# Performance work log

Measured on AMD Instinct MI355X. Metric: run time of the kernel, lower is better.

## Reference

```python
import jax, jax.numpy as jnp
import numpy as np

MLOG32 = float(np.log(32.0))


def _maxpool(x, k):
    # F.max_pool2d(stride=1, padding=k//2) pads with -inf, matching init value
    pad = k // 2
    return jax.lax.reduce_window(x, -jnp.inf, jax.lax.max, (1, 1, k, k), (1, 1, 1, 1),
                                 ((0, 0), (0, 0), (pad, pad), (pad, pad)))


def _minpool(x, k):
    return -_maxpool(-x, k)


def _local_sum(x, k):
    # conv2d with all-ones kxk kernel, zero padding, same spatial size
    pad = k // 2
    return jax.lax.reduce_window(x, 0.0, jax.lax.add, (1, 1, k, k), (1, 1, 1, 1),
                                 ((0, 0), (0, 0), (pad, pad), (pad, pad)))


def _conv3(x, kern):
    # torch conv2d == cross-correlation == lax conv (no kernel flip)
    return jax.lax.conv_general_dilated(x, kern, (1, 1), ((1, 1), (1, 1)),
                                        dimension_numbers=('NCHW', 'OIHW', 'NCHW'))


def _otsu(gray, bins=32):
    # vectorized per-batch Otsu threshold; gray in [0,1]
    B, _, H, W = gray.shape
    v = gray.reshape(B, -1)
    idx = jnp.clip((v * bins).astype(jnp.int32), 0, bins - 1)  # histc semantics, v==1 -> last bin
    hist = jax.vmap(lambda i: jnp.bincount(i, length=bins))(idx).astype(gray.dtype)
    p = hist / (H * W + 1e-6)
    xs = jnp.linspace(0.0, 1.0, bins, dtype=gray.dtype)
    omega = jnp.cumsum(p, axis=1)
    mu = jnp.cumsum(p * xs[None, :], axis=1)
    mu_t = mu[:, -1:]
    sigma_b2 = (mu_t * omega - mu) ** 2 / (omega * (1.0 - omega) + 1e-8)
    kbest = jnp.argmax(sigma_b2, axis=1)
    edges = jnp.linspace(0.0, 1.0, bins + 1, dtype=gray.dtype)
    return edges[kbest].reshape(B, 1, 1, 1)


def _concept_maps(image_rgb, cell_dilate=10, k_local=9):
    r, g, b = image_rgb[:, 0:1], image_rgb[:, 1:2], image_rgb[:, 2:3]
    gray = jnp.clip(0.5 * (0.299 * r + 0.587 * g + 0.114 * b + 1.0), 0.0, 1.0)
    thr = _otsu(gray)
    nuc = (gray <= thr).astype(gray.dtype)
    # morphological open+close, k=3
    e = _minpool(nuc, 3)
    d = _maxpool(e, 3)
    d = _maxpool(d, 3)
    e2 = _minpool(d, 3)
    nuc = (e2 > 0.5).astype(gray.dtype)
    er = _minpool(nuc, 3)
    boundary = jnp.maximum(nuc - er, 0.0)
    lap_k = jnp.array([[0, 1, 0], [1, -4, 1], [0, 1, 0]], dtype=gray.dtype).reshape(1, 1, 3, 3)
    lap = jnp.abs(_conv3(nuc, lap_k))
    den = _local_sum(boundary, 5) + 1e-6
    roughness = lap * boundary / den
    kx = jnp.array([[1, 0, -1], [2, 0, -2], [1, 0, -1]], dtype=gray.dtype).reshape(1, 1, 3, 3)
    ky = jnp.array([[1, 2, 1], [0, 0, 0], [-1, -2, -1]], dtype=gray.dtype).reshape(1, 1, 3, 3)
    gx = _conv3(gray, kx)
    gy = _conv3(gray, ky)
    ang = jnp.arctan2(gy, gx)
    den_orient = _local_sum(jnp.ones_like(gray), k_local) + 1e-6
    ms = _local_sum(jnp.sin(ang), k_local) / den_orient
    mc = _local_sum(jnp.cos(ang), k_local) / den_orient
    circ_var = 1.0 - jnp.sqrt(ms ** 2 + mc ** 2 + 1e-6)
    kd = cell_dilate if cell_dilate % 2 == 1 else cell_dilate + 1  # force odd
    cell = jnp.minimum(_maxpool(nuc, kd), 1.0)
    A_n = _local_sum(nuc, k_local)
    A_c = jnp.maximum(_local_sum(cell, k_local) - A_n, 1.0)
    nc = A_n / A_c
    g2 = _local_sum(gray * gray, k_local) / den_orient
    g1 = _local_sum(gray, k_local) / den_orient
    ent_like = jnp.log1p(jnp.maximum(g2 - g1 * g1, 0.0))
    z_maps = jnp.concatenate([roughness, circ_var, nc, ent_like], axis=1)
    return z_maps, nuc


def _energy_forward(image_rgb, cal_a, cal_b, alpha_logits, tau_p, Ht, Wt):
    z_maps, nuc = _concept_maps(image_rgb)
    z0 = jnp.log1p(jnp.maximum(z_maps[:, 0:1], 0.0))
    z1 = jnp.clip(z_maps[:, 1:2], 0.0, 1.0)
    z2 = jnp.log1p(jnp.maximum(z_maps[:, 2:3], 0.0))
    z3 = jnp.clip(z_maps[:, 3:4], 0.0, MLOG32)
    z_stable = jnp.concatenate([z0, z1, z2, z3], axis=1)
    z_cal = jax.nn.softplus(cal_a)[None, :, None, None] * z_stable + cal_b[None, :, None, None]
    alpha = jax.nn.softmax(alpha_logits)[None, :, None, None]
    E = jnp.sum(alpha * z_cal, axis=1, keepdims=True)
    B = E.shape[0]
    if (E.shape[2], E.shape[3]) != (Ht, Wt):
        E_t = jax.image.resize(E, (B, 1, Ht, Wt), method='linear')
    else:
        E_t = E
    tau = 0.2 + jax.nn.softplus(tau_p)
    A = jax.nn.softmax((-E_t / tau).reshape(B, 1, Ht * Wt), axis=-1).reshape(B, 1, Ht, Wt)
    return A, z_maps, nuc, E_t


def setup_inputs() -> dict:
    key = jax.random.key(0)
    k1, k2, k3, k4 = jax.random.split(key, 4)
    B, H, W = 16, 512, 512
    image_rgb = 2.0 * jax.random.uniform(k1, (B, 3, H, W), dtype=jnp.float32) - 1.0
    cal_a = 1.0 + 0.1 * jax.random.normal(k2, (4,), jnp.float32)
    cal_b = 0.1 * jax.random.normal(k3, (4,), jnp.float32)
    alpha_logits = 0.1 * jax.random.normal(k4, (4,), jnp.float32)
    tau_p = jnp.float32(0.5)
    return {"image_rgb": image_rgb, "cal_a": cal_a, "cal_b": cal_b,
            "alpha_logits": alpha_logits, "tau_p": tau_p, "target_h": 512, "target_w": 512}


def reference(image_rgb, cal_a, cal_b, alpha_logits, tau_p, target_h, target_w):
    return _energy_forward(image_rgb, cal_a, cal_b, alpha_logits, tau_p, int(target_h), int(target_w))
```

## Files before the change

kernel.cpp:

```cpp
#include <hip/hip_runtime.h>
#include <math.h>
#include <stdint.h>

#define HW 512
#define IMG (HW*HW)
#define MLOG32f 3.4657359027997265f

__device__ __forceinline__ float grayf(float r, float g, float b) {
    float t = __fadd_rn(__fadd_rn(__fmul_rn(0.299f, r), __fmul_rn(0.587f, g)), __fmul_rn(0.114f, b));
    float s = __fmul_rn(0.5f, __fadd_rn(t, 1.0f));
    return fminf(fmaxf(s, 0.0f), 1.0f);
}

__device__ __forceinline__ float softplusf(float x) {
    return fmaxf(x, 0.0f) + log1pf(expf(-fabsf(x)));
}

__device__ __forceinline__ float frcp(float x)  { return __builtin_amdgcn_rcpf(x); }
__device__ __forceinline__ float frsq(float x)  { return __builtin_amdgcn_rsqf(x); }
__device__ __forceinline__ float flog1p(float x){ return __logf(1.0f + x); }

__device__ __forceinline__ uint64_t kmask(int lo, int hi) {
    return (1ull << hi) - (1ull << lo);
}

__global__ __launch_bounds__(256) void k_gray_hist(const float* __restrict__ img,
                                                   float* __restrict__ gray,
                                                   int* __restrict__ hist) {
    __shared__ int lh[32];
    int tid = threadIdx.x;
    int b = blockIdx.y;
    if (tid < 32) lh[tid] = 0;
    __syncthreads();
    const float4* rp = (const float4*)(img + (size_t)b * 3 * IMG);
    const float4* gp = (const float4*)(img + (size_t)b * 3 * IMG + IMG);
    const float4* bp = (const float4*)(img + (size_t)b * 3 * IMG + 2 * IMG);
    float4* op = (float4*)(gray + (size_t)b * IMG);
    int i = blockIdx.x * 256 + tid;
    float4 r = rp[i], g = gp[i], bb = bp[i];
    float4 o;
    o.x = grayf(r.x, g.x, bb.x);
    o.y = grayf(r.y, g.y, bb.y);
    o.z = grayf(r.z, g.z, bb.z);
    o.w = grayf(r.w, g.w, bb.w);
    op[i] = o;
    int idx[4];
    idx[0] = min(max((int)(o.x * 32.0f), 0), 31);
    idx[1] = min(max((int)(o.y * 32.0f), 0), 31);
    idx[2] = min(max((int)(o.z * 32.0f), 0), 31);
    idx[3] = min(max((int)(o.w * 32.0f), 0), 31);
    int lane = tid & 63;
    int bin = lane & 31;
    int cnt = 0;
    #pragma unroll
    for (int e = 0; e < 4; e++) {
        int v = idx[e];
        unsigned long long m0 = __ballot((v & 1)  != 0);
        unsigned long long m1 = __ballot((v & 2)  != 0);
        unsigned long long m2 = __ballot((v & 4)  != 0);
        unsigned long long m3 = __ballot((v & 8)  != 0);
        unsigned long long m4 = __ballot((v & 16) != 0);
        unsigned long long mm = (bin & 1)  ? m0 : ~m0;
        mm &= (bin & 2)  ? m1 : ~m1;
        mm &= (bin & 4)  ? m2 : ~m2;
        mm &= (bin & 8)  ? m3 : ~m3;
        mm &= (bin & 16) ? m4 : ~m4;
        cnt += __popcll(mm);
    }
    if (lane < 32) atomicAdd(&lh[bin], cnt);
    __syncthreads();
    if (tid < 32) atomicAdd(&hist[b * 32 + tid], lh[tid]);
}

__global__ void k_otsu_sc(const int* __restrict__ hist,
                          const float* __restrict__ cal_a, const float* __restrict__ cal_b,
                          const float* __restrict__ alpha_logits, const float* __restrict__ tau_p,
                          float* __restrict__ thr, float* __restrict__ sc, int B) {
    int tid = threadIdx.x;
    if (tid < B) {
        const int* h = hist + tid * 32;
        float omega[32], mu[32];
        float co = 0.0f, cm = 0.0f;
        for (int k = 0; k < 32; k++) {
            float pk = (float)h[k] * (1.0f / 262144.0f);
            float xs = (float)((double)k / 31.0);
            co += pk;
            cm += pk * xs;
            omega[k] = co; mu[k] = cm;
        }
        float mu_t = mu[31];
        float best = -1e30f; int kb = 0;
        for (int k = 0; k < 32; k++) {
            float t = mu_t * omega[k] - mu[k];
            float sb = (t * t) / (omega[k] * (1.0f - omega[k]) + 1e-8f);
            if (sb > best) { best = sb; kb = k; }
        }
        thr[tid] = (float)kb * 0.03125f;
    }
    if (tid == 63) {
        float al[4];
        float m = -1e30f;
        for (int c = 0; c < 4; c++) { al[c] = alpha_logits[c]; m = fmaxf(m, al[c]); }
        float e[4]; float s = 0.0f;
        for (int c = 0; c < 4; c++) { e[c] = expf(al[c] - m); s += e[c]; }
        float bias = 0.0f;
        for (int c = 0; c < 4; c++) {
            float alpha = e[c] / s;
            sc[c] = alpha * softplusf(cal_a[c]);
            bias += alpha * cal_b[c];
        }
        sc[4] = bias;
        float tau = 0.2f + softplusf(tau_p[0]);
        sc[5] = tau;
        sc[6] = -1.0f / tau;
    }
}

__global__ __launch_bounds__(256) void k_thresh(const float* __restrict__ gray,
                                                const float* __restrict__ thr,
                                                uint32_t* __restrict__ packed) {
    int b = blockIdx.y;
    int i = blockIdx.x * 256 + threadIdx.x;
    float t = thr[b];
    float v = gray[(size_t)b * IMG + i];
    unsigned long long m = __ballot(v <= t);
    if ((threadIdx.x & 63) == 0)
        *(uint64_t*)&packed[(size_t)b * 8192 + (i >> 5)] = m;
}

__global__ __launch_bounds__(256) void k_morph(const uint32_t* __restrict__ p0,
                                               uint32_t* __restrict__ pn) {
    __shared__ uint64_t s0[40], s1[40];
    int tid = threadIdx.x, b = blockIdx.z;
    int x0 = blockIdx.x * 32, y0 = blockIdx.y * 32;
    int w0 = x0 >> 5;
    const uint32_t* pb = p0 + (size_t)b * 8192;
    int xlo = (x0 == 0) ? 4 : 0;
    int xhi = (x0 == 480) ? 36 : 40;
    uint64_t mwin = kmask(xlo, xhi);

    if (tid < 40) {
        int y = y0 - 4 + tid;
        uint64_t v = 0;
        if ((unsigned)y < (unsigned)HW) {
            const uint32_t* rowp = pb + y * 16;
            uint64_t wm = (w0 > 0)  ? rowp[w0 - 1] : 0;
            uint64_t wc = rowp[w0];
            uint64_t wp = (w0 < 15) ? rowp[w0 + 1] : 0;
            v = ((wm >> 28) | (wc << 4) | (wp << 36)) & kmask(0, 40);
        }
        s0[tid] = v;
    }
    __syncthreads();
    if (tid >= 1 && tid < 39) {
        uint64_t e = ~0ull;
        for (int dq = -1; dq <= 1; dq++) {
            int q = tid + dq;
            int y = y0 - 4 + q;
            uint64_t m = ((unsigned)y < (unsigned)HW) ? mwin : 0;
            uint64_t v = s0[q] | ~m;
            e &= v & (v << 1) & (v >> 1);
        }
        s1[tid] = e;
    }
    __syncthreads();
    if (tid >= 2 && tid < 38) {
        uint64_t d = 0;
        uint64_t me = kmask(1, 39);
        for (int dq = -1; dq <= 1; dq++) {
            int q = tid + dq;
            int y = y0 - 4 + q;
            uint64_t m = ((unsigned)y < (unsigned)HW) ? (mwin & me) : 0;
            uint64_t v = s1[q] & m;
            d |= v | (v << 1) | (v >> 1);
        }
        s0[tid] = d;
    }
    __syncthreads();
    if (tid >= 3 && tid < 37) {
        uint64_t d = 0;
        uint64_t me = kmask(2, 38);
        for (int dq = -1; dq <= 1; dq++) {
            int q = tid + dq;
            int y = y0 - 4 + q;
            uint64_t m = ((unsigned)y < (unsigned)HW) ? (mwin & me) : 0;
            uint64_t v = s0[q] & m;
            d |= v | (v << 1) | (v >> 1);
        }
        s1[tid] = d;
    }
    __syncthreads();
    if (tid >= 4 && tid < 36) {
        uint64_t e = ~0ull;
        uint64_t me = kmask(3, 37);
        for (int dq = -1; dq <= 1; dq++) {
            int q = tid + dq;
            int y = y0 - 4 + q;
            uint64_t m = ((unsigned)y < (unsigned)HW) ? (mwin & me) : 0;
            uint64_t v = s1[q] | ~m;
            e &= v & (v << 1) & (v >> 1);
        }
        s0[tid] = e;
    }
    __syncthreads();
    if (tid < 32) {
        int y = y0 + tid;
        pn[(size_t)b * 8192 + y * 16 + w0] = (uint32_t)(s0[tid + 4] >> 4);
    }
}

__global__ __launch_bounds__(256) void k_maps(const float* __restrict__ gray,
                                              const uint32_t* __restrict__ pn,
                                              float* __restrict__ zmap,
                                              float* __restrict__ nucf,
                                              float* __restrict__ Eout,
                                              const float* __restrict__ sc,
                                              float* __restrict__ expsum) {
    __shared__ __align__(16) char smem[30912];
    __shared__ uint64_t nrow[50], ehr[50], dilh[50], bnd[36], cell[40];
    float* gt  = (float*)smem;
    float* st  = (float*)(smem + 7232);
    float* ct  = (float*)(smem + 13792);
    float* rs0 = (float*)(smem + 20352);
    float* rs1 = (float*)(smem + 25632);
    int* rs_n = (int*)smem;
    int* rs_c = (int*)(smem + 5120);
    int* rs_b = (int*)(smem + 10240);
    float* red = (float*)(smem + 16384);

    int tid = threadIdx.x, b = blockIdx.z;
    int x0 = blockIdx.x * 32, y0 = blockIdx.y * 32;
    int w0 = x0 >> 5;
    const float* gb = gray + (size_t)b * IMG;
    const uint32_t* pb = pn + (size_t)b * 8192;
    int xlo = (x0 == 0) ? 9 : 0;
    int xhi = (x0 == 480) ? 41 : 50;
    uint64_t mwin = kmask(xlo, xhi);

    for (int i = tid; i < 42 * 42; i += 256) {
        int ly = i / 42, lx = i % 42;
        int gy = y0 + ly - 5, gx = x0 + lx - 5;
        gt[ly * 43 + lx] = (gy >= 0 && gy < HW && gx >= 0 && gx < HW) ? gb[gy * HW + gx] : 0.0f;
    }
    if (tid < 50) {
        int y = y0 - 9 + tid;
        uint64_t v = 0;
        if ((unsigned)y < (unsigned)HW) {
            const uint32_t* rowp = pb + y * 16;
            uint64_t wm = (w0 > 0)  ? rowp[w0 - 1] : 0;
            uint64_t wc = rowp[w0];
            uint64_t wp = (w0 < 15) ? rowp[w0 + 1] : 0;
            v = ((wm >> 23) | (wc << 9) | (wp << 41)) & kmask(0, 50);
        }
        nrow[tid] = v;
    }
    __syncthreads();

    if (tid < 50) {
        uint64_t v = nrow[tid];
        uint64_t d = v | (v << 1) | (v >> 1);
        d = d | (d << 2) | (d >> 2);
        d = d | (d << 2) | (d >> 2);
        dilh[tid] = d;
    }
    if (tid >= 6 && tid < 44) {
        int y = y0 - 9 + tid;
        uint64_t m = ((unsigned)y < (unsigned)HW) ? mwin : 0;
        uint64_t v = nrow[tid] | ~m;
        ehr[tid] = v & (v << 1) & (v >> 1);
    }
    for (int i = tid; i < 1600; i += 256) {
        int ly = i / 40, lx = i % 40;
        int gy = y0 + ly - 4, gx = x0 + lx - 4;
        float s = 0.0f, c = 0.0f;
        if (gy >= 0 && gy < HW && gx >= 0 && gx < HW) {
            float a00 = gt[ly * 43 + lx],       a01 = gt[ly * 43 + lx + 1],       a02 = gt[ly * 43 + lx + 2];
            float a10 = gt[(ly + 1) * 43 + lx],                                   a12 = gt[(ly + 1) * 43 + lx + 2];
            float a20 = gt[(ly + 2) * 43 + lx], a21 = gt[(ly + 2) * 43 + lx + 1], a22 = gt[(ly + 2) * 43 + lx + 2];
            float gxv = (a00 - a02) + 2.0f * (a10 - a12) + (a20 - a22);
            float gyv = (a00 + 2.0f * a01 + a02) - (a20 + 2.0f * a21 + a22);
            float r2 = gxv * gxv + gyv * gyv;
            if (r2 > 0.0f) { float ir = frsq(r2); s = gyv * ir; c = gxv * ir; }
            else { s = 0.0f; c = 1.0f; }
        }
        st[ly * 41 + lx] = s; ct[ly * 41 + lx] = c;
    }
    __syncthreads();

    if (tid < 36) {
        int r = tid + 7;
        uint64_t er = ehr[r - 1] & ehr[r] & ehr[r + 1];
        bnd[tid] = nrow[r] & ~er;
    }
    if (tid < 40) {
        int r = tid + 5;
        int y = y0 - 4 + tid;
        uint64_t c = 0;
        for (int d = -5; d <= 5; d++) c |= dilh[r + d];
        uint64_t m = ((unsigned)y < (unsigned)HW) ? mwin : 0;
        cell[tid] = c & m;
    }
    for (int i = tid; i < 320; i += 256) {
        int ly = i >> 3, c0 = (i & 7) << 2;
        int base = ly * 41 + c0;
        float sa[12], ca[12];
        #pragma unroll
        for (int j = 0; j < 12; j++) { sa[j] = st[base + j]; ca[j] = ct[base + j]; }
        float ss = sa[0]+sa[1]+sa[2]+sa[3]+sa[4]+sa[5]+sa[6]+sa[7]+sa[8];
        float cs = ca[0]+ca[1]+ca[2]+ca[3]+ca[4]+ca[5]+ca[6]+ca[7]+ca[8];
        int ob = ly * 33 + c0;
        rs0[ob] = ss; rs1[ob] = cs;
        #pragma unroll
        for (int q = 1; q < 4; q++) {
            ss += sa[8 + q] - sa[q - 1];
            cs += ca[8 + q] - ca[q - 1];
            rs0[ob + q] = ss; rs1[ob + q] = cs;
        }
    }
    __syncthreads();

    int p = tid & 31, py0 = (tid >> 5) << 2;
    int gx = x0 + p;
    float cntx = (float)(min(gx + 4, HW - 1) - max(gx - 4, 0) + 1);
    float z1v[4], z3v[4];
    {
        float s[12], c[12];
        #pragma unroll
        for (int j = 0; j < 12; j++) { s[j] = rs0[(py0 + j) * 33 + p]; c[j] = rs1[(py0 + j) * 33 + p]; }
        float ss = s[0]+s[1]+s[2]+s[3]+s[4]+s[5]+s[6]+s[7]+s[8];
        float cs = c[0]+c[1]+c[2]+c[3]+c[4]+c[5]+c[6]+c[7]+c[8];
        #pragma unroll
        for (int q = 0; q < 4; q++) {
            int gy = y0 + py0 + q;
            float cnty = (float)(min(gy + 4, HW - 1) - max(gy - 4, 0) + 1);
            float iden = frcp(cnty * cntx + 1e-6f);
            float ms = ss * iden, mc = cs * iden;
            z1v[q] = 1.0f - sqrtf(ms * ms + mc * mc + 1e-6f);
            if (q < 3) { ss += s[9 + q] - s[q]; cs += c[9 + q] - c[q]; }
        }
    }
    __syncthreads();

    for (int i = tid; i < 320; i += 256) {
        int ly = i >> 3, c0 = (i & 7) << 2;
        int base = (ly + 1) * 43 + c0 + 1;
        float v[12];
        #pragma unroll
        for (int j = 0; j < 12; j++) v[j] = gt[base + j];
        float gs = v[0]+v[1]+v[2]+v[3]+v[4]+v[5]+v[6]+v[7]+v[8];
        float g2 = v[0]*v[0]+v[1]*v[1]+v[2]*v[2]+v[3]*v[3]+v[4]*v[4]+v[5]*v[5]+v[6]*v[6]+v[7]*v[7]+v[8]*v[8];
        int ob = ly * 33 + c0;
        rs0[ob] = gs; rs1[ob] = g2;
        #pragma unroll
        for (int q = 1; q < 4; q++) {
            gs += v[8 + q] - v[q - 1];
            g2 += v[8 + q] * v[8 + q] - v[q - 1] * v[q - 1];
            rs0[ob + q] = gs; rs1[ob + q] = g2;
        }
    }
    __syncthreads();

    {
        float s[12], c[12];
        #pragma unroll
        for (int j = 0; j < 12; j++) { s[j] = rs0[(py0 + j) * 33 + p]; c[j] = rs1[(py0 + j) * 33 + p]; }
        float gs = s[0]+s[1]+s[2]+s[3]+s[4]+s[5]+s[6]+s[7]+s[8];
        float g2 = c[0]+c[1]+c[2]+c[3]+c[4]+c[5]+c[6]+c[7]+c[8];
        #pragma unroll
        for (int q = 0; q < 4; q++) {
            int gy = y0 + py0 + q;
            float cnty = (float)(min(gy + 4, HW - 1) - max(gy - 4, 0) + 1);
            float iden = frcp(cnty * cntx + 1e-6f);
            float g1 = gs * iden, gq = g2 * iden;
            z3v[q] = flog1p(fmaxf(gq - g1 * g1, 0.0f));
            if (q < 3) { gs += s[9 + q] - s[q]; g2 += c[9 + q] - c[q]; }
        }
    }
    __syncthreads();

    for (int i = tid; i < 40 * 32; i += 256) {
        int rr = i >> 5, pp = i & 31;
        rs_n[rr * 32 + pp] = __popcll((nrow[rr + 5] >> (pp + 5)) & 0x1FFull);
        rs_c[rr * 32 + pp] = __popcll((cell[rr]     >> (pp + 5)) & 0x1FFull);
    }
    for (int i = tid; i < 36 * 32; i += 256) {
        int rr = i >> 5, pp = i & 31;
        rs_b[rr * 32 + pp] = __popcll((bnd[rr] >> (pp + 7)) & 0x1Full);
    }
    __syncthreads();

    float w0f = sc[0], w1f = sc[1], w2f = sc[2], w3f = sc[3], bias = sc[4], ntau = sc[6];
    float* z0p = zmap + ((size_t)b * 4 + 0) * IMG;
    float* z1p = zmap + ((size_t)b * 4 + 1) * IMG;
    float* z2p = zmap + ((size_t)b * 4 + 2) * IMG;
    float* z3p = zmap + ((size_t)b * 4 + 3) * IMG;
    float* Ep  = Eout + (size_t)b * IMG;
    float* np  = nucf + (size_t)b * IMG;
    float acc = 0.0f;
    {
        int nn[12], cc[12], bb8[8];
        #pragma unroll
        for (int j = 0; j < 12; j++) { nn[j] = rs_n[(py0 + j) * 32 + p]; cc[j] = rs_c[(py0 + j) * 32 + p]; }
        #pragma unroll
        for (int j = 0; j < 8; j++) bb8[j] = rs_b[(py0 + j) * 32 + p];
        int An = nn[0]+nn[1]+nn[2]+nn[3]+nn[4]+nn[5]+nn[6]+nn[7]+nn[8];
        int Ac = cc[0]+cc[1]+cc[2]+cc[3]+cc[4]+cc[5]+cc[6]+cc[7]+cc[8];
        int db = bb8[0]+bb8[1]+bb8[2]+bb8[3]+bb8[4];
        int kk = p + 9;
        #pragma unroll
        for (int q = 0; q < 4; q++) {
            int py = py0 + q;
            int r = py + 9;
            uint64_t rowc = nrow[r];
            int cbit = (int)((rowc >> kk) & 1);
            int nb4  = (int)((nrow[r - 1] >> kk) & 1) + (int)((nrow[r + 1] >> kk) & 1)
                     + (int)((rowc >> (kk - 1)) & 1) + (int)((rowc >> (kk + 1)) & 1);
            int lap = nb4 - 4 * cbit; lap = lap < 0 ? -lap : lap;
            int bc  = (int)((bnd[py + 2] >> kk) & 1);
            float rough = (float)(lap * bc) * frcp((float)db + 1e-6f);
            float z2 = (float)An * frcp(fmaxf((float)(Ac - An), 1.0f));
            float z0s = flog1p(fmaxf(rough, 0.0f));
            float z1s = fminf(fmaxf(z1v[q], 0.0f), 1.0f);
            float z2s = flog1p(fmaxf(z2, 0.0f));
            float z3s = fminf(fmaxf(z3v[q], 0.0f), MLOG32f);
            float E = w0f * z0s + w1f * z1s + w2f * z2s + w3f * z3s + bias;
            int gy = y0 + py;
            size_t o = (size_t)gy * HW + x0 + p;
            z0p[o] = rough;
            z1p[o] = z1v[q];
            z2p[o] = z2;
            z3p[o] = z3v[q];
            Ep[o]  = E;
            np[o]  = (float)cbit;
            acc += __expf(E * ntau);
            if (q < 3) {
                An += nn[9 + q] - nn[q];
                Ac += cc[9 + q] - cc[q];
                db += bb8[5 + q] - bb8[q];
            }
        }
    }
    for (int off = 32; off > 0; off >>= 1) acc += __shfl_down(acc, off, 64);
    if ((tid & 63) == 0) red[tid >> 6] = acc;
    __syncthreads();
    if (tid == 0) atomicAdd(&expsum[b], red[0] + red[1] + red[2] + red[3]);
}

__global__ __launch_bounds__(256) void k_softmaxA(const float* __restrict__ E,
                                                  float* __restrict__ A,
                                                  const float* __restrict__ sc,
                                                  const float* __restrict__ expsum) {
    int b = blockIdx.y;
    int i = blockIdx.x * 256 + threadIdx.x;
    float ntau = sc[6];
    float invS = 1.0f / expsum[b];
    const float4* Ep = (const float4*)(E + (size_t)b * IMG);
    float4* Ap = (float4*)(A + (size_t)b * IMG);
    float4 e = Ep[i];
    float4 o;
    o.x = __expf(e.x * ntau) * invS;
    o.y = __expf(e.y * ntau) * invS;
    o.z = __expf(e.z * ntau) * invS;
    o.w = __expf(e.w * ntau) * invS;
    Ap[i] = o;
}

extern "C" void kernel_launch(void* const* d_in, const int* in_sizes, int n_in,
                              void* d_out, int out_size, void* d_ws, size_t ws_size,
                              hipStream_t stream) {
    const float* img   = (const float*)d_in[0];
    const float* cal_a = (const float*)d_in[1];
    const float* cal_b = (const float*)d_in[2];
    const float* alpha = (const float*)d_in[3];
    const float* tau_p = (const float*)d_in[4];
    int B = in_sizes[0] / (3 * IMG);

    float* out  = (float*)d_out;
    float* A    = out;
    float* zmap = out + (size_t)B * IMG;
    float* nuc  = out + (size_t)B * IMG * 5;
    float* E    = out + (size_t)B * IMG * 6;
    float* gray = A;

    int*      hist    = (int*)d_ws;
    float*    expsum  = (float*)d_ws + B * 32;
    float*    thr     = expsum + B;
    float*    sc      = thr + B;
    uint32_t* packed0 = (uint32_t*)d_ws + 1024;
    uint32_t* packedN = packed0 + (size_t)B * 8192;

    hipMemsetAsync(d_ws, 0, (size_t)(B * 32 + B) * 4, stream);
    k_gray_hist<<<dim3(IMG / 1024, B), 256, 0, stream>>>(img, gray, hist);
    k_otsu_sc<<<1, 64, 0, stream>>>(hist, cal_a, cal_b, alpha, tau_p, thr, sc, B);
    k_thresh<<<dim3(IMG / 256, B), 256, 0, stream>>>(gray, thr, packed0);
    dim3 tg(HW / 32, HW / 32, B);
    k_morph<<<tg, 256, 0, stream>>>(packed0, packedN);
    k_maps<<<tg, 256, 0, stream>>>(gray, packedN, zmap, nuc, E, sc, expsum);
    k_softmaxA<<<dim3(IMG / 1024, B), 256, 0, stream>>>(E, A, sc, expsum);
}
```

Measured before the change: 247.8 us.

## Fuse all stages into one persistent cooperative kernel with grid syncs

Result: slower. 459.1 us (+85.3%).

```diff
diff --git a/kernel.cpp b/kernel.cpp
--- a/kernel.cpp
+++ b/kernel.cpp
@@ -1,6 +1,9 @@
 #include <hip/hip_runtime.h>
+#include <hip/hip_cooperative_groups.h>
 #include <math.h>
 #include <stdint.h>
+
+namespace cg = cooperative_groups;
 
 #define HW 512
 #define IMG (HW*HW)
@@ -24,198 +27,15 @@
     return (1ull << hi) - (1ull << lo);
 }
 
-__global__ __launch_bounds__(256) void k_gray_hist(const float* __restrict__ img,
-                                                   float* __restrict__ gray,
-                                                   int* __restrict__ hist) {
-    __shared__ int lh[32];
-    int tid = threadIdx.x;
-    int b = blockIdx.y;
-    if (tid < 32) lh[tid] = 0;
-    __syncthreads();
-    const float4* rp = (const float4*)(img + (size_t)b * 3 * IMG);
-    const float4* gp = (const float4*)(img + (size_t)b * 3 * IMG + IMG);
-    const float4* bp = (const float4*)(img + (size_t)b * 3 * IMG + 2 * IMG);
-    float4* op = (float4*)(gray + (size_t)b * IMG);
-    int i = blockIdx.x * 256 + tid;
-    float4 r = rp[i], g = gp[i], bb = bp[i];
-    float4 o;
-    o.x = grayf(r.x, g.x, bb.x);
-    o.y = grayf(r.y, g.y, bb.y);
-    o.z = grayf(r.z, g.z, bb.z);
-    o.w = grayf(r.w, g.w, bb.w);
-    op[i] = o;
-    int idx[4];
-    idx[0] = min(max((int)(o.x * 32.0f), 0), 31);
-    idx[1] = min(max((int)(o.y * 32.0f), 0), 31);
-    idx[2] = min(max((int)(o.z * 32.0f), 0), 31);
-    idx[3] = min(max((int)(o.w * 32.0f), 0), 31);
-    int lane = tid & 63;
-    int bin = lane & 31;
-    int cnt = 0;
-    #pragma unroll
-    for (int e = 0; e < 4; e++) {
-        int v = idx[e];
-        unsigned long long m0 = __ballot((v & 1)  != 0);
-        unsigned long long m1 = __ballot((v & 2)  != 0);
-        unsigned long long m2 = __ballot((v & 4)  != 0);
-        unsigned long long m3 = __ballot((v & 8)  != 0);
-        unsigned long long m4 = __ballot((v & 16) != 0);
-        unsigned long long mm = (bin & 1)  ? m0 : ~m0;
-        mm &= (bin & 2)  ? m1 : ~m1;
-        mm &= (bin & 4)  ? m2 : ~m2;
-        mm &= (bin & 8)  ? m3 : ~m3;
-        mm &= (bin & 16) ? m4 : ~m4;
-        cnt += __popcll(mm);
-    }
-    if (lane < 32) atomicAdd(&lh[bin], cnt);
-    __syncthreads();
-    if (tid < 32) atomicAdd(&hist[b * 32 + tid], lh[tid]);
-}
-
-__global__ void k_otsu_sc(const int* __restrict__ hist,
-                          const float* __restrict__ cal_a, const float* __restrict__ cal_b,
-                          const float* __restrict__ alpha_logits, const float* __restrict__ tau_p,
-                          float* __restrict__ thr, float* __restrict__ sc, int B) {
-    int tid = threadIdx.x;
-    if (tid < B) {
-        const int* h = hist + tid * 32;
-        float omega[32], mu[32];
-        float co = 0.0f, cm = 0.0f;
-        for (int k = 0; k < 32; k++) {
-            float pk = (float)h[k] * (1.0f / 262144.0f);
-            float xs = (float)((double)k / 31.0);
-            co += pk;
-            cm += pk * xs;
-            omega[k] = co; mu[k] = cm;
-        }
-        float mu_t = mu[31];
-        float best = -1e30f; int kb = 0;
-        for (int k = 0; k < 32; k++) {
-            float t = mu_t * omega[k] - mu[k];
-            float sb = (t * t) / (omega[k] * (1.0f - omega[k]) + 1e-8f);
-            if (sb > best) { best = sb; kb = k; }
-        }
-        thr[tid] = (float)kb * 0.03125f;
-    }
-    if (tid == 63) {
-        float al[4];
-        float m = -1e30f;
-        for (int c = 0; c < 4; c++) { al[c] = alpha_logits[c]; m = fmaxf(m, al[c]); }
-        float e[4]; float s = 0.0f;
-        for (int c = 0; c < 4; c++) { e[c] = expf(al[c] - m); s += e[c]; }
-        float bias = 0.0f;
-        for (int c = 0; c < 4; c++) {
-            float alpha = e[c] / s;
-            sc[c] = alpha * softplusf(cal_a[c]);
-            bias += alpha * cal_b[c];
-        }
-        sc[4] = bias;
-        float tau = 0.2f + softplusf(tau_p[0]);
-        sc[5] = tau;
-        sc[6] = -1.0f / tau;
-    }
-}
-
-__global__ __launch_bounds__(256) void k_thresh(const float* __restrict__ gray,
-                                                const float* __restrict__ thr,
-                                                uint32_t* __restrict__ packed) {
-    int b = blockIdx.y;
-    int i = blockIdx.x * 256 + threadIdx.x;
-    float t = thr[b];
-    float v = gray[(size_t)b * IMG + i];
-    unsigned long long m = __ballot(v <= t);
-    if ((threadIdx.x & 63) == 0)
-        *(uint64_t*)&packed[(size_t)b * 8192 + (i >> 5)] = m;
-}
-
-__global__ __launch_bounds__(256) void k_morph(const uint32_t* __restrict__ p0,
-                                               uint32_t* __restrict__ pn) {
-    __shared__ uint64_t s0[40], s1[40];
-    int tid = threadIdx.x, b = blockIdx.z;
-    int x0 = blockIdx.x * 32, y0 = blockIdx.y * 32;
-    int w0 = x0 >> 5;
-    const uint32_t* pb = p0 + (size_t)b * 8192;
-    int xlo = (x0 == 0) ? 4 : 0;
-    int xhi = (x0 == 480) ? 36 : 40;
-    uint64_t mwin = kmask(xlo, xhi);
-
-    if (tid < 40) {
-        int y = y0 - 4 + tid;
-        uint64_t v = 0;
-        if ((unsigned)y < (unsigned)HW) {
-            const uint32_t* rowp = pb + y * 16;
-            uint64_t wm = (w0 > 0)  ? rowp[w0 - 1] : 0;
-            uint64_t wc = rowp[w0];
-            uint64_t wp = (w0 < 15) ? rowp[w0 + 1] : 0;
-            v = ((wm >> 28) | (wc << 4) | (wp << 36)) & kmask(0, 40);
-        }
-        s0[tid] = v;
-    }
-    __syncthreads();
-    if (tid >= 1 && tid < 39) {
-        uint64_t e = ~0ull;
-        for (int dq = -1; dq <= 1; dq++) {
-            int q = tid + dq;
-            int y = y0 - 4 + q;
-            uint64_t m = ((unsigned)y < (unsigned)HW) ? mwin : 0;
-            uint64_t v = s0[q] | ~m;
-            e &= v & (v << 1) & (v >> 1);
-        }
-        s1[tid] = e;
-    }
-    __syncthreads();
-    if (tid >= 2 && tid < 38) {
-        uint64_t d = 0;
-        uint64_t me = kmask(1, 39);
-        for (int dq = -1; dq <= 1; dq++) {
-            int q = tid + dq;
-            int y = y0 - 4 + q;
-            uint64_t m = ((unsigned)y < (unsigned)HW) ? (mwin & me) : 0;
-            uint64_t v = s1[q] & m;
-            d |= v | (v << 1) | (v >> 1);
-        }
-        s0[tid] = d;
-    }
-    __syncthreads();
-    if (tid >= 3 && tid < 37) {
-        uint64_t d = 0;
-        uint64_t me = kmask(2, 38);
-        for (int dq = -1; dq <= 1; dq++) {
-            int q = tid + dq;
-            int y = y0 - 4 + q;
-            uint64_t m = ((unsigned)y < (unsigned)HW) ? (mwin & me) : 0;
-            uint64_t v = s0[q] & m;
-            d |= v | (v << 1) | (v >> 1);
-        }
-        s1[tid] = d;
-    }
-    __syncthreads();
-    if (tid >= 4 && tid < 36) {
-        uint64_t e = ~0ull;
-        uint64_t me = kmask(3, 37);
-        for (int dq = -1; dq <= 1; dq++) {
-            int q = tid + dq;
-            int y = y0 - 4 + q;
-            uint64_t m = ((unsigned)y < (unsigned)HW) ? (mwin & me) : 0;
-            uint64_t v = s1[q] | ~m;
-            e &= v & (v << 1) & (v >> 1);
-        }
-        s0[tid] = e;
-    }
-    __syncthreads();
-    if (tid < 32) {
-        int y = y0 + tid;
-        pn[(size_t)b * 8192 + y * 16 + w0] = (uint32_t)(s0[tid + 4] >> 4);
-    }
-}
-
-__global__ __launch_bounds__(256) void k_maps(const float* __restrict__ gray,
-                                              const uint32_t* __restrict__ pn,
-                                              float* __restrict__ zmap,
-                                              float* __restrict__ nucf,
-                                              float* __restrict__ Eout,
-                                              const float* __restrict__ sc,
-                                              float* __restrict__ expsum) {
+__global__ void __launch_bounds__(256, 4)
+k_mega(const float* __restrict__ img, float* __restrict__ gray, int* __restrict__ hist,
+       uint32_t* __restrict__ pn, float* __restrict__ zmap, float* __restrict__ nucf,
+       float* __restrict__ Eout, float* __restrict__ Aout,
+       const float* __restrict__ cal_a, const float* __restrict__ cal_b,
+       const float* __restrict__ alpha_logits, const float* __restrict__ tau_p,
+       float* __restrict__ expsum, int B) {
+    cg::grid_group grid = cg::this_grid();
+
     __shared__ __align__(16) char smem[30912];
     __shared__ uint64_t nrow[50], ehr[50], dilh[50], bnd[36], cell[40];
     float* gt  = (float*)smem;
@@ -227,242 +47,407 @@
     int* rs_c = (int*)(smem + 5120);
     int* rs_b = (int*)(smem + 10240);
     float* red = (float*)(smem + 16384);
-
-    int tid = threadIdx.x, b = blockIdx.z;
-    int x0 = blockIdx.x * 32, y0 = blockIdx.y * 32;
-    int w0 = x0 >> 5;
-    const float* gb = gray + (size_t)b * IMG;
-    const uint32_t* pb = pn + (size_t)b * 8192;
-    int xlo = (x0 == 0) ? 9 : 0;
-    int xhi = (x0 == 480) ? 41 : 50;
-    uint64_t mwin = kmask(xlo, xhi);
-
-    for (int i = tid; i < 42 * 42; i += 256) {
-        int ly = i / 42, lx = i % 42;
-        int gy = y0 + ly - 5, gx = x0 + lx - 5;
-        gt[ly * 43 + lx] = (gy >= 0 && gy < HW && gx >= 0 && gx < HW) ? gb[gy * HW + gx] : 0.0f;
+    uint64_t* s0m = (uint64_t*)smem;
+    uint64_t* s1m = s0m + 40;
+
+    int tid = threadIdx.x;
+    int lane = tid & 63, wv = tid >> 6;
+    int nChunks = B * 64;
+    int nTiles  = B * 256;
+
+    float w0f, w1f, w2f, w3f, bias, ntau;
+    {
+        float al[4];
+        float m = -1e30f;
+        #pragma unroll
+        for (int c = 0; c < 4; c++) { al[c] = alpha_logits[c]; m = fmaxf(m, al[c]); }
+        float e[4]; float s = 0.0f;
+        #pragma unroll
+        for (int c = 0; c < 4; c++) { e[c] = expf(al[c] - m); s += e[c]; }
+        float w[4]; bias = 0.0f;
+        #pragma unroll
+        for (int c = 0; c < 4; c++) {
+            float alpha = e[c] / s;
+            w[c] = alpha * softplusf(cal_a[c]);
+            bias += alpha * cal_b[c];
+        }
+        w0f = w[0]; w1f = w[1]; w2f = w[2]; w3f = w[3];
+        float tau = 0.2f + softplusf(tau_p[0]);
+        ntau = -1.0f / tau;
     }
-    if (tid < 50) {
-        int y = y0 - 9 + tid;
-        uint64_t v = 0;
-        if ((unsigned)y < (unsigned)HW) {
-            const uint32_t* rowp = pb + y * 16;
-            uint64_t wm = (w0 > 0)  ? rowp[w0 - 1] : 0;
-            uint64_t wc = rowp[w0];
-            uint64_t wp = (w0 < 15) ? rowp[w0 + 1] : 0;
-            v = ((wm >> 23) | (wc << 9) | (wp << 41)) & kmask(0, 50);
-        }
-        nrow[tid] = v;
+
+    for (int ch = blockIdx.x; ch < nChunks; ch += gridDim.x) {
+        int b = ch >> 6;
+        int f4base = (ch & 63) * 1024;
+        const float4* rp = (const float4*)(img + (size_t)b * 3 * IMG) + f4base;
+        const float4* gp = (const float4*)(img + (size_t)b * 3 * IMG + IMG) + f4base;
+        const float4* bp = (const float4*)(img + (size_t)b * 3 * IMG + 2 * IMG) + f4base;
+        float4* op = (float4*)(gray + (size_t)b * IMG) + f4base;
+        int bin = lane & 31;
+        int cnt = 0;
+        #pragma unroll
+        for (int it = 0; it < 4; it++) {
+            int i = it * 256 + tid;
+            float4 r = rp[i], g = gp[i], bb = bp[i];
+            float4 o;
+            o.x = grayf(r.x, g.x, bb.x);
+            o.y = grayf(r.y, g.y, bb.y);
+            o.z = grayf(r.z, g.z, bb.z);
+            o.w = grayf(r.w, g.w, bb.w);
+            op[i] = o;
+            int idx[4];
+            idx[0] = min(max((int)(o.x * 32.0f), 0), 31);
+            idx[1] = min(max((int)(o.y * 32.0f), 0), 31);
+            idx[2] = min(max((int)(o.z * 32.0f), 0), 31);
+            idx[3] = min(max((int)(o.w * 32.0f), 0), 31);
+            #pragma unroll
+            for (int e = 0; e < 4; e++) {
+                int v = idx[e];
+                unsigned long long m0 = __ballot((v & 1)  != 0);
+                unsigned long long m1 = __ballot((v & 2)  != 0);
+                unsigned long long m2 = __ballot((v & 4)  != 0);
+                unsigned long long m3 = __ballot((v & 8)  != 0);
+                unsigned long long m4 = __ballot((v & 16) != 0);
+                unsigned long long mm = (bin & 1)  ? m0 : ~m0;
+                mm &= (bin & 2)  ? m1 : ~m1;
+                mm &= (bin & 4)  ? m2 : ~m2;
+                mm &= (bin & 8)  ? m3 : ~m3;
+                mm &= (bin & 16) ? m4 : ~m4;
+                cnt += __popcll(mm);
+            }
+        }
+        if (lane < 32) atomicAdd(&hist[b * 32 + bin], cnt);
     }
-    __syncthreads();
-
-    if (tid < 50) {
-        uint64_t v = nrow[tid];
-        uint64_t d = v | (v << 1) | (v >> 1);
-        d = d | (d << 2) | (d >> 2);
-        d = d | (d << 2) | (d >> 2);
-        dilh[tid] = d;
+    grid.sync();
+
+    for (int tile = blockIdx.x; tile < nTiles; tile += gridDim.x) {
+        int b = tile >> 8, ti = tile & 255;
+        int y0 = (ti >> 4) << 5, x0 = (ti & 15) << 5;
+        int w0 = x0 >> 5;
+        const int* h = hist + b * 32;
+        float mu_t = 0.0f;
+        #pragma unroll
+        for (int k = 0; k < 32; k++) {
+            float pk = (float)h[k] * (1.0f / 262144.0f);
+            float xs = (float)((double)k / 31.0);
+            mu_t += pk * xs;
+        }
+        float co = 0.0f, cm = 0.0f, best = -1e30f; int kb = 0;
+        #pragma unroll
+        for (int k = 0; k < 32; k++) {
+            float pk = (float)h[k] * (1.0f / 262144.0f);
+            float xs = (float)((double)k / 31.0);
+            co += pk; cm += pk * xs;
+            float t = mu_t * co - cm;
+            float sb = (t * t) / (co * (1.0f - co) + 1e-8f);
+            if (sb > best) { best = sb; kb = k; }
+        }
+        float thrv = (float)kb * 0.03125f;
+
+        const float* gb = gray + (size_t)b * IMG;
+        for (int r = wv; r < 40; r += 4) {
+            int gy = y0 - 4 + r, gx = x0 - 4 + lane;
+            bool pred = false;
+            if (lane < 40 && (unsigned)gy < (unsigned)HW && (unsigned)gx < (unsigned)HW)
+                pred = gb[gy * HW + gx] <= thrv;
+            unsigned long long m = __ballot(pred);
+            if (lane == 0) s0m[r] = m;
+        }
+        __syncthreads();
+        int xlo = (x0 == 0) ? 4 : 0;
+        int xhi = (x0 == 480) ? 36 : 40;
+        uint64_t mwin = kmask(xlo, xhi);
+        if (tid >= 1 && tid < 39) {
+            uint64_t e = ~0ull;
+            for (int dq = -1; dq <= 1; dq++) {
+                int q = tid + dq;
+                int y = y0 - 4 + q;
+                uint64_t m = ((unsigned)y < (unsigned)HW) ? mwin : 0;
+                uint64_t v = s0m[q] | ~m;
+                e &= v & (v << 1) & (v >> 1);
+            }
+            s1m[tid] = e;
+        }
+        __syncthreads();
+        if (tid >= 2 && tid < 38) {
+            uint64_t d = 0;
+            uint64_t me = kmask(1, 39);
+            for (int dq = -1; dq <= 1; dq++) {
+                int q = tid + dq;
+                int y = y0 - 4 + q;
+                uint64_t m = ((unsigned)y < (unsigned)HW) ? (mwin & me) : 0;
+                uint64_t v = s1m[q] & m;
+                d |= v | (v << 1) | (v >> 1);
+            }
+            s0m[tid] = d;
+        }
+        __syncthreads();
+        if (tid >= 3 && tid < 37) {
+            uint64_t d = 0;
+            uint64_t me = kmask(2, 38);
+            for (int dq = -1; dq <= 1; dq++) {
+                int q = tid + dq;
+                int y = y0 - 4 + q;
+                uint64_t m = ((unsigned)y < (unsigned)HW) ? (mwin & me) : 0;
+                uint64_t v = s0m[q] & m;
+                d |= v | (v << 1) | (v >> 1);
+            }
+            s1m[tid] = d;
+        }
+        __syncthreads();
+        if (tid >= 4 && tid < 36) {
+            uint64_t e = ~0ull;
+            uint64_t me = kmask(3, 37);
+            for (int dq = -1; dq <= 1; dq++) {
+                int q = tid + dq;
+                int y = y0 - 4 + q;
+                uint64_t m = ((unsigned)y < (unsigned)HW) ? (mwin & me) : 0;
+                uint64_t v = s1m[q] | ~m;
+                e &= v & (v << 1) & (v >> 1);
+            }
+            s0m[tid] = e;
+        }
+        __syncthreads();
+        if (tid < 32) {
+            int y = y0 + tid;
+            pn[(size_t)b * 8192 + y * 16 + w0] = (uint32_t)(s0m[tid + 4] >> 4);
+        }
+        __syncthreads();
     }
-    if (tid >= 6 && tid < 44) {
-        int y = y0 - 9 + tid;
-        uint64_t m = ((unsigned)y < (unsigned)HW) ? mwin : 0;
-        uint64_t v = nrow[tid] | ~m;
-        ehr[tid] = v & (v << 1) & (v >> 1);
+    grid.sync();
+
+    int p = tid & 31, py0 = (tid >> 5) << 2;
+    for (int tile = blockIdx.x; tile < nTiles; tile += gridDim.x) {
+        int b = tile >> 8, ti = tile & 255;
+        int y0 = (ti >> 4) << 5, x0 = (ti & 15) << 5;
+        int w0 = x0 >> 5;
+        const float* gb = gray + (size_t)b * IMG;
+        const uint32_t* pb = pn + (size_t)b * 8192;
+        int xlo = (x0 == 0) ? 9 : 0;
+        int xhi = (x0 == 480) ? 41 : 50;
+        uint64_t mwin = kmask(xlo, xhi);
+
+        for (int i = tid; i < 42 * 42; i += 256) {
+            int ly = i / 42, lx = i % 42;
+            int gy = y0 + ly - 5, gx = x0 + lx - 5;
+            gt[ly * 43 + lx] = (gy >= 0 && gy < HW && gx >= 0 && gx < HW) ? gb[gy * HW + gx] : 0.0f;
+        }
+        if (tid < 50) {
+            int y = y0 - 9 + tid;
+            uint64_t v = 0;
+            if ((unsigned)y < (unsigned)HW) {
+                const uint32_t* rowp = pb + y * 16;
+                uint64_t wm = (w0 > 0)  ? rowp[w0 - 1] : 0;
+                uint64_t wc = rowp[w0];
+                uint64_t wp = (w0 < 15) ? rowp[w0 + 1] : 0;
+                v = ((wm >> 23) | (wc << 9) | (wp << 41)) & kmask(0, 50);
+            }
+            nrow[tid] = v;
+        }
+        __syncthreads();
+
+        if (tid < 50) {
+            uint64_t v = nrow[tid];
+            uint64_t d = v | (v << 1) | (v >> 1);
+            d = d | (d << 2) | (d >> 2);
+            d = d | (d << 2) | (d >> 2);
+            dilh[tid] = d;
+        }
+        if (tid >= 6 && tid < 44) {
+            int y = y0 - 9 + tid;
+            uint64_t m = ((unsigned)y < (unsigned)HW) ? mwin : 0;
+            uint64_t v = nrow[tid] | ~m;
+            ehr[tid] = v & (v << 1) & (v >> 1);
+        }
+        for (int i = tid; i < 1600; i += 256) {
+            int ly = i / 40, lx = i % 40;
+            int gy = y0 + ly - 4, gx = x0 + lx - 4;
+            float s = 0.0f, c = 0.0f;
+            if (gy >= 0 && gy < HW && gx >= 0 && gx < HW) {
+                float a00 = gt[ly * 43 + lx],       a01 = gt[ly * 43 + lx + 1],       a02 = gt[ly * 43 + lx + 2];
+                float a10 = gt[(ly + 1) * 43 + lx],                                   a12 = gt[(ly + 1) * 43 + lx + 2];
+                float a20 = gt[(ly + 2) * 43 + lx], a21 = gt[(ly + 2) * 43 + lx + 1], a22 = gt[(ly + 2) * 43 + lx + 2];
+                float gxv = (a00 - a02) + 2.0f * (a10 - a12) + (a20 - a22);
+                float gyv = (a00 + 2.0f * a01 + a02) - (a20 + 2.0f * a21 + a22);
+                float r2 = gxv * gxv + gyv * gyv;
+                if (r2 > 0.0f) { float ir = frsq(r2); s = gyv * ir; c = gxv * ir; }
+                else { s = 0.0f; c = 1.0f; }
+            }
+            st[ly * 41 + lx] = s; ct[ly * 41 + lx] = c;
+        }
+        __syncthreads();
+
+        if (tid < 36) {
+            int r = tid + 7;
+            uint64_t er = ehr[r - 1] & ehr[r] & ehr[r + 1];
+            bnd[tid] = nrow[r] & ~er;
+        }
+        if (tid < 40) {
+            int r = tid + 5;
+            int y = y0 - 4 + tid;
+            uint64_t c = 0;
+            for (int d = -5; d <= 5; d++) c |= dilh[r + d];
+            uint64_t m = ((unsigned)y < (unsigned)HW) ? mwin : 0;
+            cell[tid] = c & m;
+        }
+        for (int i = tid; i < 320; i += 256) {
+            int ly = i >> 3, c0 = (i & 7) << 2;
+            int base = ly * 41 + c0;
+            float sa[12], ca[12];
+            #pragma unroll
+            for (int j = 0; j < 12; j++) { sa[j] = st[base + j]; ca[j] = ct[base + j]; }
+            float ss = sa[0]+sa[1]+sa[2]+sa[3]+sa[4]+sa[5]+sa[6]+sa[7]+sa[8];
+            float cs = ca[0]+ca[1]+ca[2]+ca[3]+ca[4]+ca[5]+ca[6]+ca[7]+ca[8];
+            int ob = ly * 33 + c0;
+            rs0[ob] = ss; rs1[ob] = cs;
+            #pragma unroll
+            for (int q = 1; q < 4; q++) {
+                ss += sa[8 + q] - sa[q - 1];
+                cs += ca[8 + q] - ca[q - 1];
+                rs0[ob + q] = ss; rs1[ob + q] = cs;
+            }
+        }
+        __syncthreads();
+
+        int gx = x0 + p;
+        float cntx = (float)(min(gx + 4, HW - 1) - max(gx - 4, 0) + 1);
+        float z1v[4], z3v[4];
+        {
+            float s[12], c[12];
+            #pragma unroll
+            for (int j = 0; j < 12; j++) { s[j] = rs0[(py0 + j) * 33 + p]; c[j] = rs1[(py0 + j) * 33 + p]; }
+            float ss = s[0]+s[1]+s[2]+s[3]+s[4]+s[5]+s[6]+s[7]+s[8];
+            float cs = c[0]+c[1]+c[2]+c[3]+c[4]+c[5]+c[6]+c[7]+c[8];
+            #pragma unroll
+            for (int q = 0; q < 4; q++) {
+                int gy = y0 + py0 + q;
+                float cnty = (float)(min(gy + 4, HW - 1) - max(gy - 4, 0) + 1);
+                float iden = frcp(cnty * cntx + 1e-6f);
+                float ms = ss * iden, mc = cs * iden;
+                z1v[q] = 1.0f - sqrtf(ms * ms + mc * mc + 1e-6f);
+                if (q < 3) { ss += s[9 + q] - s[q]; cs += c[9 + q] - c[q]; }
+            }
+        }
+        __syncthreads();
+
+        for (int i = tid; i < 320; i += 256) {
+            int ly = i >> 3, c0 = (i & 7) << 2;
+            int base = (ly + 1) * 43 + c0 + 1;
+            float v[12];
+            #pragma unroll
+            for (int j = 0; j < 12; j++) v[j] = gt[base + j];
+            float gs = v[0]+v[1]+v[2]+v[3]+v[4]+v[5]+v[6]+v[7]+v[8];
+            float g2 = v[0]*v[0]+v[1]*v[1]+v[2]*v[2]+v[3]*v[3]+v[4]*v[4]+v[5]*v[5]+v[6]*v[6]+v[7]*v[7]+v[8]*v[8];
+            int ob = ly * 33 + c0;
+            rs0[ob] = gs; rs1[ob] = g2;
+            #pragma unroll
+            for (int q = 1; q < 4; q++) {
+                gs += v[8 + q] - v[q - 1];
+                g2 += v[8 + q] * v[8 + q] - v[q - 1] * v[q - 1];
+                rs0[ob + q] = gs; rs1[ob + q] = g2;
+            }
+        }
+        __syncthreads();
+
+        {
+            float s[12], c[12];
+            #pragma unroll
+            for (int j = 0; j < 12; j++) { s[j] = rs0[(py0 + j) * 33 + p]; c[j] = rs1[(py0 + j) * 33 + p]; }
+            float gs = s[0]+s[1]+s[2]+s[3]+s[4]+s[5]+s[6]+s[7]+s[8];
+            float g2 = c[0]+c[1]+c[2]+c[3]+c[4]+c[5]+c[6]+c[7]+c[8];
+            #pragma unroll
+            for (int q = 0; q < 4; q++) {
+                int gy = y0 + py0 + q;
+                float cnty = (float)(min(gy + 4, HW - 1) - max(gy - 4, 0) + 1);
+                float iden = frcp(cnty * cntx + 1e-6f);
+                float g1 = gs * iden, gq = g2 * iden;
+                z3v[q] = flog1p(fmaxf(gq - g1 * g1, 0.0f));
+                if (q < 3) { gs += s[9 + q] - s[q]; g2 += c[9 + q] - c[q]; }
+            }
+        }
+        __syncthreads();
+
+        for (int i = tid; i < 40 * 32; i += 256) {
+            int rr = i >> 5, pp = i & 31;
+            rs_n[rr * 32 + pp] = __popcll((nrow[rr + 5] >> (pp + 5)) & 0x1FFull);
+            rs_c[rr * 32 + pp] = __popcll((cell[rr]     >> (pp + 5)) & 0x1FFull);
+        }
+        for (int i = tid; i < 36 * 32; i += 256) {
+            int rr = i >> 5, pp = i & 31;
+            rs_b[rr * 32 + pp] = __popcll((bnd[rr] >> (pp + 7)) & 0x1Full);
+        }
+        __syncthreads();
+
+        float* z0p = zmap + ((size_t)b * 4 + 0) * IMG;
+        float* z1p = zmap + ((size_t)b * 4 + 1) * IMG;
+        float* z2p = zmap + ((size_t)b * 4 + 2) * IMG;
+        float* z3p = zmap + ((size_t)b * 4 + 3) * IMG;
+        float* Ep  = Eout + (size_t)b * IMG;
+        float* np  = nucf + (size_t)b * IMG;
+        float acc = 0.0f;
+        {
+            int nn[12], cc[12], bb8[8];
+            #pragma unroll
+            for (int j = 0; j < 12; j++) { nn[j] = rs_n[(py0 + j) * 32 + p]; cc[j] = rs_c[(py0 + j) * 32 + p]; }
+            #pragma unroll
+            for (int j = 0; j < 8; j++) bb8[j] = rs_b[(py0 + j) * 32 + p];
+            int An = nn[0]+nn[1]+nn[2]+nn[3]+nn[4]+nn[5]+nn[6]+nn[7]+nn[8];
+            int Ac = cc[0]+cc[1]+cc[2]+cc[3]+cc[4]+cc[5]+cc[6]+cc[7]+cc[8];
+            int db = bb8[0]+bb8[1]+bb8[2]+bb8[3]+bb8[4];
+            int kk = p + 9;
+            #pragma unroll
+            for (int q = 0; q < 4; q++) {
+                int py = py0 + q;
+                int r = py + 9;
+                uint64_t rowc = nrow[r];
+                int cbit = (int)((rowc >> kk) & 1);
+                int nb4  = (int)((nrow[r - 1] >> kk) & 1) + (int)((nrow[r + 1] >> kk) & 1)
+                         + (int)((rowc >> (kk - 1)) & 1) + (int)((rowc >> (kk + 1)) & 1);
+                int lap = nb4 - 4 * cbit; lap = lap < 0 ? -lap : lap;
+                int bc  = (int)((bnd[py + 2] >> kk) & 1);
+                float rough = (float)(lap * bc) * frcp((float)db + 1e-6f);
+                float z2 = (float)An * frcp(fmaxf((float)(Ac - An), 1.0f));
+                float z0s = flog1p(fmaxf(rough, 0.0f));
+                float z1s = fminf(fmaxf(z1v[q], 0.0f), 1.0f);
+                float z2s = flog1p(fmaxf(z2, 0.0f));
+                float z3s = fminf(fmaxf(z3v[q], 0.0f), MLOG32f);
+                float E = w0f * z0s + w1f * z1s + w2f * z2s + w3f * z3s + bias;
+                int gy = y0 + py;
+                size_t o = (size_t)gy * HW + x0 + p;
+                z0p[o] = rough;
+                z1p[o] = z1v[q];
+                z2p[o] = z2;
+                z3p[o] = z3v[q];
+                Ep[o]  = E;
+                np[o]  = (float)cbit;
+                acc += __expf(E * ntau);
+                if (q < 3) {
+                    An += nn[9 + q] - nn[q];
+                    Ac += cc[9 + q] - cc[q];
+                    db += bb8[5 + q] - bb8[q];
+                }
+            }
+        }
+        for (int off = 32; off > 0; off >>= 1) acc += __shfl_down(acc, off, 64);
+        if (lane == 0) red[wv] = acc;
+        __syncthreads();
+        if (tid == 0) atomicAdd(&expsum[b], red[0] + red[1] + red[2] + red[3]);
+        __syncthreads();
     }
-    for (int i = tid; i < 1600; i += 256) {
-        int ly = i / 40, lx = i % 40;
-        int gy = y0 + ly - 4, gx = x0 + lx - 4;
-        float s = 0.0f, c = 0.0f;
-        if (gy >= 0 && gy < HW && gx >= 0 && gx < HW) {
-            float a00 = gt[ly * 43 + lx],       a01 = gt[ly * 43 + lx + 1],       a02 = gt[ly * 43 + lx + 2];
-            float a10 = gt[(ly + 1) * 43 + lx],                                   a12 = gt[(ly + 1) * 43 + lx + 2];
-            float a20 = gt[(ly + 2) * 43 + lx], a21 = gt[(ly + 2) * 43 + lx + 1], a22 = gt[(ly + 2) * 43 + lx + 2];
-            float gxv = (a00 - a02) + 2.0f * (a10 - a12) + (a20 - a22);
-            float gyv = (a00 + 2.0f * a01 + a02) - (a20 + 2.0f * a21 + a22);
-            float r2 = gxv * gxv + gyv * gyv;
-            if (r2 > 0.0f) { float ir = frsq(r2); s = gyv * ir; c = gxv * ir; }
-            else { s = 0.0f; c = 1.0f; }
-        }
-        st[ly * 41 + lx] = s; ct[ly * 41 + lx] = c;
+    grid.sync();
+
+    int nF4 = B * (IMG / 4);
+    for (int j = blockIdx.x * 256 + tid; j < nF4; j += gridDim.x * 256) {
+        int b = j >> 16;
+        float invS = 1.0f / expsum[b];
+        float4 e = ((const float4*)Eout)[j];
+        float4 o;
+        o.x = __expf(e.x * ntau) * invS;
+        o.y = __expf(e.y * ntau) * invS;
+        o.z = __expf(e.z * ntau) * invS;
+        o.w = __expf(e.w * ntau) * invS;
+        ((float4*)Aout)[j] = o;
     }
-    __syncthreads();
-
-    if (tid < 36) {
-        int r = tid + 7;
-        uint64_t er = ehr[r - 1] & ehr[r] & ehr[r + 1];
-        bnd[tid] = nrow[r] & ~er;
-    }
-    if (tid < 40) {
-        int r = tid + 5;
-        int y = y0 - 4 + tid;
-        uint64_t c = 0;
-        for (int d = -5; d <= 5; d++) c |= dilh[r + d];
-        uint64_t m = ((unsigned)y < (unsigned)HW) ? mwin : 0;
-        cell[tid] = c & m;
-    }
-    for (int i = tid; i < 320; i += 256) {
-        int ly = i >> 3, c0 = (i & 7) << 2;
-        int base = ly * 41 + c0;
-        float sa[12], ca[12];
-        #pragma unroll
-        for (int j = 0; j < 12; j++) { sa[j] = st[base + j]; ca[j] = ct[base + j]; }
-        float ss = sa[0]+sa[1]+sa[2]+sa[3]+sa[4]+sa[5]+sa[6]+sa[7]+sa[8];
-        float cs = ca[0]+ca[1]+ca[2]+ca[3]+ca[4]+ca[5]+ca[6]+ca[7]+ca[8];
-        int ob = ly * 33 + c0;
-        rs0[ob] = ss; rs1[ob] = cs;
-        #pragma unroll
-        for (int q = 1; q < 4; q++) {
-            ss += sa[8 + q] - sa[q - 1];
-            cs += ca[8 + q] - ca[q - 1];
-            rs0[ob + q] = ss; rs1[ob + q] = cs;
-        }
-    }
-    __syncthreads();
-
-    int p = tid & 31, py0 = (tid >> 5) << 2;
-    int gx = x0 + p;
-    float cntx = (float)(min(gx + 4, HW - 1) - max(gx - 4, 0) + 1);
-    float z1v[4], z3v[4];
-    {
-        float s[12], c[12];
-        #pragma unroll
-        for (int j = 0; j < 12; j++) { s[j] = rs0[(py0 + j) * 33 + p]; c[j] = rs1[(py0 + j) * 33 + p]; }
-        float ss = s[0]+s[1]+s[2]+s[3]+s[4]+s[5]+s[6]+s[7]+s[8];
-        float cs = c[0]+c[1]+c[2]+c[3]+c[4]+c[5]+c[6]+c[7]+c[8];
-        #pragma unroll
-        for (int q = 0; q < 4; q++) {
-            int gy = y0 + py0 + q;
-            float cnty = (float)(min(gy + 4, HW - 1) - max(gy - 4, 0) + 1);
-            float iden = frcp(cnty * cntx + 1e-6f);
-            float ms = ss * iden, mc = cs * iden;
-            z1v[q] = 1.0f - sqrtf(ms * ms + mc * mc + 1e-6f);
-            if (q < 3) { ss += s[9 + q] - s[q]; cs += c[9 + q] - c[q]; }
-        }
-    }
-    __syncthreads();
-
-    for (int i = tid; i < 320; i += 256) {
-        int ly = i >> 3, c0 = (i & 7) << 2;
-        int base = (ly + 1) * 43 + c0 + 1;
-        float v[12];
-        #pragma unroll
-        for (int j = 0; j < 12; j++) v[j] = gt[base + j];
-        float gs = v[0]+v[1]+v[2]+v[3]+v[4]+v[5]+v[6]+v[7]+v[8];
-        float g2 = v[0]*v[0]+v[1]*v[1]+v[2]*v[2]+v[3]*v[3]+v[4]*v[4]+v[5]*v[5]+v[6]*v[6]+v[7]*v[7]+v[8]*v[8];
-        int ob = ly * 33 + c0;
-        rs0[ob] = gs; rs1[ob] = g2;
-        #pragma unroll
-        for (int q = 1; q < 4; q++) {
-            gs += v[8 + q] - v[q - 1];
-            g2 += v[8 + q] * v[8 + q] - v[q - 1] * v[q - 1];
-            rs0[ob + q] = gs; rs1[ob + q] = g2;
-        }
-    }
-    __syncthreads();
-
-    {
-        float s[12], c[12];
-        #pragma unroll
-        for (int j = 0; j < 12; j++) { s[j] = rs0[(py0 + j) * 33 + p]; c[j] = rs1[(py0 + j) * 33 + p]; }
-        float gs = s[0]+s[1]+s[2]+s[3]+s[4]+s[5]+s[6]+s[7]+s[8];
-        float g2 = c[0]+c[1]+c[2]+c[3]+c[4]+c[5]+c[6]+c[7]+c[8];
-        #pragma unroll
-        for (int q = 0; q < 4; q++) {
-            int gy = y0 + py0 + q;
-            float cnty = (float)(min(gy + 4, HW - 1) - max(gy - 4, 0) + 1);
-            float iden = frcp(cnty * cntx + 1e-6f);
-            float g1 = gs * iden, gq = g2 * iden;
-            z3v[q] = flog1p(fmaxf(gq - g1 * g1, 0.0f));
-            if (q < 3) { gs += s[9 + q] - s[q]; g2 += c[9 + q] - c[q]; }
-        }
-    }
-    __syncthreads();
-
-    for (int i = tid; i < 40 * 32; i += 256) {
-        int rr = i >> 5, pp = i & 31;
-        rs_n[rr * 32 + pp] = __popcll((nrow[rr + 5] >> (pp + 5)) & 0x1FFull);
-        rs_c[rr * 32 + pp] = __popcll((cell[rr]     >> (pp + 5)) & 0x1FFull);
-    }
-    for (int i = tid; i < 36 * 32; i += 256) {
-        int rr = i >> 5, pp = i & 31;
-        rs_b[rr * 32 + pp] = __popcll((bnd[rr] >> (pp + 7)) & 0x1Full);
-    }
-    __syncthreads();
-
-    float w0f = sc[0], w1f = sc[1], w2f = sc[2], w3f = sc[3], bias = sc[4], ntau = sc[6];
-    float* z0p = zmap + ((size_t)b * 4 + 0) * IMG;
-    float* z1p = zmap + ((size_t)b * 4 + 1) * IMG;
-    float* z2p = zmap + ((size_t)b * 4 + 2) * IMG;
-    float* z3p = zmap + ((size_t)b * 4 + 3) * IMG;
-    float* Ep  = Eout + (size_t)b * IMG;
-    float* np  = nucf + (size_t)b * IMG;
-    float acc = 0.0f;
-    {
-        int nn[12], cc[12], bb8[8];
-        #pragma unroll
-        for (int j = 0; j < 12; j++) { nn[j] = rs_n[(py0 + j) * 32 + p]; cc[j] = rs_c[(py0 + j) * 32 + p]; }
-        #pragma unroll
-        for (int j = 0; j < 8; j++) bb8[j] = rs_b[(py0 + j) * 32 + p];
-        int An = nn[0]+nn[1]+nn[2]+nn[3]+nn[4]+nn[5]+nn[6]+nn[7]+nn[8];
-        int Ac = cc[0]+cc[1]+cc[2]+cc[3]+cc[4]+cc[5]+cc[6]+cc[7]+cc[8];
-        int db = bb8[0]+bb8[1]+bb8[2]+bb8[3]+bb8[4];
-        int kk = p + 9;
-        #pragma unroll
-        for (int q = 0; q < 4; q++) {
-            int py = py0 + q;
-            int r = py + 9;
-            uint64_t rowc = nrow[r];
-            int cbit = (int)((rowc >> kk) & 1);
-            int nb4  = (int)((nrow[r - 1] >> kk) & 1) + (int)((nrow[r + 1] >> kk) & 1)
-                     + (int)((rowc >> (kk - 1)) & 1) + (int)((rowc >> (kk + 1)) & 1);
-            int lap = nb4 - 4 * cbit; lap = lap < 0 ? -lap : lap;
-            int bc  = (int)((bnd[py + 2] >> kk) & 1);
-            float rough = (float)(lap * bc) * frcp((float)db + 1e-6f);
-            float z2 = (float)An * frcp(fmaxf((float)(Ac - An), 1.0f));
-            float z0s = flog1p(fmaxf(rough, 0.0f));
-            float z1s = fminf(fmaxf(z1v[q], 0.0f), 1.0f);
-            float z2s = flog1p(fmaxf(z2, 0.0f));
-            float z3s = fminf(fmaxf(z3v[q], 0.0f), MLOG32f);
-            float E = w0f * z0s + w1f * z1s + w2f * z2s + w3f * z3s + bias;
-            int gy = y0 + py;
-            size_t o = (size_t)gy * HW + x0 + p;
-            z0p[o] = rough;
-            z1p[o] = z1v[q];
-            z2p[o] = z2;
-            z3p[o] = z3v[q];
-            Ep[o]  = E;
-            np[o]  = (float)cbit;
-            acc += __expf(E * ntau);
-            if (q < 3) {
-                An += nn[9 + q] - nn[q];
-                Ac += cc[9 + q] - cc[q];
-                db += bb8[5 + q] - bb8[q];
-            }
-        }
-    }
-    for (int off = 32; off > 0; off >>= 1) acc += __shfl_down(acc, off, 64);
-    if ((tid & 63) == 0) red[tid >> 6] = acc;
-    __syncthreads();
-    if (tid == 0) atomicAdd(&expsum[b], red[0] + red[1] + red[2] + red[3]);
-}
-
-__global__ __launch_bounds__(256) void k_softmaxA(const float* __restrict__ E,
-                                                  float* __restrict__ A,
-                                                  const float* __restrict__ sc,
-                                                  const float* __restrict__ expsum) {
-    int b = blockIdx.y;
-    int i = blockIdx.x * 256 + threadIdx.x;
-    float ntau = sc[6];
-    float invS = 1.0f / expsum[b];
-    const float4* Ep = (const float4*)(E + (size_t)b * IMG);
-    float4* Ap = (float4*)(A + (size_t)b * IMG);
-    float4 e = Ep[i];
-    float4 o;
-    o.x = __expf(e.x * ntau) * invS;
-    o.y = __expf(e.y * ntau) * invS;
-    o.z = __expf(e.z * ntau) * invS;
-    o.w = __expf(e.w * ntau) * invS;
-    Ap[i] = o;
 }
 
 extern "C" void kernel_launch(void* const* d_in, const int* in_sizes, int n_in,
@@ -484,17 +469,19 @@
 
     int*      hist    = (int*)d_ws;
     float*    expsum  = (float*)d_ws + B * 32;
-    float*    thr     = expsum + B;
-    float*    sc      = thr + B;
-    uint32_t* packed0 = (uint32_t*)d_ws + 1024;
-    uint32_t* packedN = packed0 + (size_t)B * 8192;
+    uint32_t* packedN = (uint32_t*)((char*)d_ws + 4096);
 
     hipMemsetAsync(d_ws, 0, (size_t)(B * 32 + B) * 4, stream);
-    k_gray_hist<<<dim3(IMG / 1024, B), 256, 0, stream>>>(img, gray, hist);
-    k_otsu_sc<<<1, 64, 0, stream>>>(hist, cal_a, cal_b, alpha, tau_p, thr, sc, B);
-    k_thresh<<<dim3(IMG / 256, B), 256, 0, stream>>>(gray, thr, packed0);
-    dim3 tg(HW / 32, HW / 32, B);
-    k_morph<<<tg, 256, 0, stream>>>(packed0, packedN);
-    k_maps<<<tg, 256, 0, stream>>>(gray, packedN, zmap, nuc, E, sc, expsum);
-    k_softmaxA<<<dim3(IMG / 1024, B), 256, 0, stream>>>(E, A, sc, expsum);
+
+    int maxB = 0;
+    hipOccupancyMaxActiveBlocksPerMultiprocessor(&maxB, k_mega, 256, 0);
+    if (maxB < 1) maxB = 1;
+    int G = maxB * 256;
+    if (G > B * 64) G = B * 64;
+
+    void* args[] = {(void*)&img, (void*)&gray, (void*)&hist, (void*)&packedN,
+                    (void*)&zmap, (void*)&nuc, (void*)&E, (void*)&A,
+                    (void*)&cal_a, (void*)&cal_b, (void*)&alpha, (void*)&tau_p,
+                    (void*)&expsum, (void*)&B};
+    hipLaunchCooperativeKernel((void*)k_mega, dim3(G), dim3(256), args, 0, stream);
 }
```
